# Optimization experiments

Hardware: AMD Instinct MI355X
Metric: run time of the kernel (lower is better)

## Reference

```python
import jax, jax.numpy as jnp
import numpy as np

NUM_HEADS = 16

def rotate_half(x):
    x1, x2 = jnp.split(x, 2, axis=-1)
    return jnp.concatenate((-x2, x1), axis=-1)

def setup_inputs() -> dict:
    key = jax.random.key(0)
    ks = jax.random.split(key, 5)
    b, n, dim, hd = 2, 2048, 1024, 64
    return {
        "x": jax.random.normal(ks[0], (b, n, dim), dtype=jnp.float32),
        "Wqkv": jax.random.normal(ks[1], (3 * dim, dim), dtype=jnp.float32) * (dim ** -0.5),
        "Wproj": jax.random.normal(ks[2], (dim, dim), dtype=jnp.float32) * (dim ** -0.5),
        "bproj": jnp.zeros((dim,), dtype=jnp.float32),
        "sin": jax.random.normal(ks[3], (n, hd), dtype=jnp.float32),
        "cos": jax.random.normal(ks[4], (n, hd), dtype=jnp.float32),
    }

def reference(x, Wqkv, Wproj, bproj, sin, cos):
    b, n, dim = x.shape
    h = NUM_HEADS
    d = dim // h
    qkv = x @ Wqkv.T
    qkv = qkv.reshape(b, n, 3, h, d).transpose(2, 0, 3, 1, 4)
    q, k, v = qkv[0], qkv[1], qkv[2]
    # RoPE: sin/cos [n, d] broadcast over [b, h, n, d]
    q = q * cos + rotate_half(q) * sin
    k = k * cos + rotate_half(k) * sin
    # SDPA (non-causal, no dropout at eval)
    scale = d ** -0.5
    scores = jnp.einsum("bhnd,bhmd->bhnm", q, k) * scale
    attn = jax.nn.softmax(scores, axis=-1)
    out = jnp.einsum("bhnm,bhmd->bhnd", attn, v)
    # merge heads: [b, h, n, d] -> [b, n, h*d]
    out = out.transpose(0, 2, 1, 3).reshape(b, n, dim)
    return out @ Wproj.T + bproj
```

## Files before the change

### kernel.cpp

```cpp
#include <hip/hip_runtime.h>
#include <hip/hip_fp16.h>

typedef _Float16 f16;
typedef _Float16 half8 __attribute__((ext_vector_type(8)));
typedef _Float16 half4v __attribute__((ext_vector_type(4)));
typedef __fp16 fp16x2 __attribute__((ext_vector_type(2)));
typedef float f32x4 __attribute__((ext_vector_type(4)));

#define QSCALE 0.18033688011112042f
#define SHIFT2 17.312340490667560f

__device__ __forceinline__ void gload_lds16(const void* g, void* lds) {
  __builtin_amdgcn_global_load_lds(
      (__attribute__((address_space(1))) void*)g,
      (__attribute__((address_space(3))) void*)lds, 16, 0, 0);
}

__global__ __launch_bounds__(256) void cvt_all_kernel(
    const float* __restrict__ x, const float* __restrict__ wqkv,
    const float* __restrict__ wproj, f16* __restrict__ xh,
    f16* __restrict__ wqkvh, f16* __restrict__ wprojh) {
  int i = blockIdx.x * 256 + threadIdx.x;
  const float* src; f16* dst; int off;
  if (i < 1048576)      { src = x;     dst = xh;     off = i; }
  else if (i < 1835008) { src = wqkv;  dst = wqkvh;  off = i - 1048576; }
  else                  { src = wproj; dst = wprojh; off = i - 1835008; }
  float4 v = ((const float4*)src)[off];
  half4v o;
  o.x = (f16)v.x; o.y = (f16)v.y; o.z = (f16)v.z; o.w = (f16)v.w;
  ((half4v*)dst)[off] = o;
}

template<int EPI, int VAR>
__global__ __launch_bounds__(256) void hgemm_kernel(
    const f16* __restrict__ A16, const f16* __restrict__ B, int K, int yoff,
    const float* __restrict__ cosT, const float* __restrict__ sinT,
    f16* __restrict__ Qout, f16* __restrict__ Kout, f16* __restrict__ Vtout,
    const float* __restrict__ bias, float* __restrict__ Cout) {
  constexpr int BN = (EPI == 0) ? 128 : 64;
  constexpr int NJ = (EPI == 0) ? 4 : 2;
  constexpr int NBUF = (VAR == 0) ? 2 : 3;
  __shared__ f16 As[NBUF][128 * 32];
  __shared__ f16 Bs[NBUF][BN * 32];
  const int tid = threadIdx.x;
  const int lane = tid & 63, w = tid >> 6;
  const int fr = lane & 15, fkg = lane >> 4;
  const int wm = (w >> 1) * 64;
  const int wn = (EPI == 0) ? (w & 1) * 64 : (w & 1) * 16;
  const long long rowBase = (long long)blockIdx.x * 128;
  const long long colBase = (long long)(blockIdx.y + yoff) * BN;

  f32x4 acc[4][NJ] = {};
  const f16* Ab = A16 + rowBase * K;
  const f16* Bb = B + colBase * K;

  const int srow = lane >> 2;
  const int kcol = ((lane & 3) ^ ((lane >> 3) & 3)) * 8;
  const int sw = (fkg ^ ((fr >> 1) & 3)) * 8;

  auto stage = [&](int buf, int k0) {
#pragma unroll
    for (int r = 0; r < 2; ++r) {
      int c = r * 4 + w;
      gload_lds16(Ab + (long long)(c * 16 + srow) * K + k0 + kcol, &As[buf][c * 512]);
    }
    if (EPI == 0) {
#pragma unroll
      for (int r = 0; r < 2; ++r) {
        int c = r * 4 + w;
        gload_lds16(Bb + (long long)(c * 16 + srow) * K + k0 + kcol, &Bs[buf][c * 512]);
      }
    } else {
      int c = w;
      gload_lds16(Bb + (long long)(c * 16 + srow) * K + k0 + kcol, &Bs[buf][c * 512]);
    }
  };

  const int NT = K >> 5;
  stage(0, 0);
  stage(1, 32);
  if (VAR == 0) {
    for (int t = 0; t < NT; ++t) {
      const int buf = t & 1;
      const int k0 = t << 5;
      if (t + 1 < NT) {
        if constexpr (EPI == 0) asm volatile("s_waitcnt vmcnt(4)" ::: "memory");
        else                    asm volatile("s_waitcnt vmcnt(3)" ::: "memory");
      } else {
        asm volatile("s_waitcnt vmcnt(0)" ::: "memory");
      }
      __builtin_amdgcn_s_barrier();
      __builtin_amdgcn_sched_barrier(0);
      half8 a[4], b[NJ];
#pragma unroll
      for (int i = 0; i < 4; ++i)
        a[i] = *(const half8*)(&As[buf][((wm >> 4) + i) * 512 + fr * 32 + sw]);
#pragma unroll
      for (int j = 0; j < NJ; ++j) {
        int chunk = (EPI == 0) ? ((wn >> 4) + j) : ((wn >> 4) + j * 2);
        b[j] = *(const half8*)(&Bs[buf][chunk * 512 + fr * 32 + sw]);
      }
      asm volatile("s_waitcnt lgkmcnt(0)" ::: "memory");
      __builtin_amdgcn_sched_barrier(0);
      __builtin_amdgcn_s_barrier();
      if (t + 2 < NT) stage(buf, k0 + 64);
#pragma unroll
      for (int i = 0; i < 4; ++i)
#pragma unroll
        for (int j = 0; j < NJ; ++j)
          acc[i][j] = __builtin_amdgcn_mfma_f32_16x16x32_f16(a[i], b[j], acc[i][j], 0, 0, 0);
    }
  } else {
    int bcur = 0, bst = 2;
    for (int t = 0; t < NT; ++t) {
      if (t + 1 < NT) {
        if constexpr (EPI == 0) asm volatile("s_waitcnt vmcnt(4)" ::: "memory");
        else                    asm volatile("s_waitcnt vmcnt(3)" ::: "memory");
      } else {
        asm volatile("s_waitcnt vmcnt(0)" ::: "memory");
      }
      __builtin_amdgcn_s_barrier();
      __builtin_amdgcn_sched_barrier(0);
      if (t + 2 < NT) stage(bst, (t + 2) << 5);
      half8 a[4], b[NJ];
#pragma unroll
      for (int i = 0; i < 4; ++i)
        a[i] = *(const half8*)(&As[bcur][((wm >> 4) + i) * 512 + fr * 32 + sw]);
#pragma unroll
      for (int j = 0; j < NJ; ++j) {
        int chunk = (EPI == 0) ? ((wn >> 4) + j) : ((wn >> 4) + j * 2);
        b[j] = *(const half8*)(&Bs[bcur][chunk * 512 + fr * 32 + sw]);
      }
#pragma unroll
      for (int i = 0; i < 4; ++i)
#pragma unroll
        for (int j = 0; j < NJ; ++j)
          acc[i][j] = __builtin_amdgcn_mfma_f32_16x16x32_f16(a[i], b[j], acc[i][j], 0, 0, 0);
      bcur = (bcur == 2) ? 0 : bcur + 1;
      bst  = (bst == 2) ? 0 : bst + 1;
    }
  }

  if (EPI == 0) {
#pragma unroll
    for (int i = 0; i < 4; ++i) {
#pragma unroll
      for (int r = 0; r < 4; ++r) {
        int rg = (int)rowBase + wm + i * 16 + fkg * 4 + r;
        int bidx = rg >> 11, nn = rg & 2047;
#pragma unroll
        for (int j = 0; j < 4; ++j) {
          int cg = (int)colBase + wn + j * 16 + fr;
          int t = cg >> 10, cc = cg & 1023;
          int head = cc >> 6, d = cc & 63;
          int bh = bidx * 16 + head;
          float v = acc[i][j][r];
          if (t == 2) {
            Vtout[((long long)bh * 64 + d) * 2048 + nn] = (f16)v;
          } else {
            float pal = acc[i][j ^ 2][r];
            float cs = cosT[nn * 64 + d];
            float sn = sinT[nn * 64 + d];
            v = v * cs + (d < 32 ? -pal : pal) * sn;
            if (t == 0) v *= QSCALE;
            f16 hv = (f16)v;
            if (t == 0) Qout[((long long)bh * 2048 + nn) * 64 + d] = hv;
            else        Kout[((long long)bh * 2048 + nn) * 64 + d] = hv;
          }
        }
      }
    }
  } else {
#pragma unroll
    for (int i = 0; i < 4; ++i)
#pragma unroll
      for (int r = 0; r < 4; ++r) {
        long long rg = rowBase + wm + i * 16 + fkg * 4 + r;
#pragma unroll
        for (int j = 0; j < NJ; ++j) {
          int cg = (int)colBase + wn + j * 32 + fr;
          Cout[rg * 1024 + cg] = acc[i][j][r] + bias[cg];
        }
      }
  }
}

__global__ __launch_bounds__(256) void attn_kernel(
    const f16* __restrict__ Q, const f16* __restrict__ Kb,
    const f16* __restrict__ Vt, f16* __restrict__ Om) {
  __shared__ f16 Ks[2][64 * 64];
  __shared__ f16 Vs[2][64 * 64];
  const int tid = threadIdx.x;
  const int lane = tid & 63, w = tid >> 6;
  const int fr = lane & 15, fkg = lane >> 4, fk = fkg * 8;

  const int lin = blockIdx.x;
  const int slot = lin >> 3;
  const int bh = (lin & 7) * 4 + (slot >> 4);
  const int q0 = (slot & 15) * 128 + w * 32;

  const f16* Kbh = Kb + (long long)bh * 2048 * 64;
  const f16* Vbh = Vt + (long long)bh * 64 * 2048;

  half8 aq[2][2];
#pragma unroll
  for (int m = 0; m < 2; ++m)
#pragma unroll
    for (int ks = 0; ks < 2; ++ks)
      aq[m][ks] = *(const half8*)(Q + ((long long)bh * 2048 + q0 + m * 16 + fr) * 64 +
                                  ks * 32 + fk);

  half8 ones_frag;
#pragma unroll
  for (int j = 0; j < 8; ++j) ones_frag[j] = (fr == 0) ? (f16)1.0f : (f16)0.0f;

  f32x4 acc[2][4] = {};
  f32x4 accL[2] = {};

  const int srow = lane >> 3;
  const int ssub = ((lane & 7) ^ srow) * 8;
  long long koff[2], voff[2];
  int ldst[2];
#pragma unroll
  for (int c = 0; c < 2; ++c) {
    int R = w * 16 + c * 8 + srow;
    int pr = (R & 0x23) | ((R & 0x0C) << 1) | ((R & 0x10) >> 2);
    koff[c] = (long long)pr * 64 + ssub;
    voff[c] = (long long)R * 2048 + ssub;
    ldst[c] = (w * 16 + c * 8) * 64;
  }
  const f16* kpt = Kbh;
  const f16* vpt = Vbh;

  auto stage = [&](int buf) {
#pragma unroll
    for (int c = 0; c < 2; ++c) {
      gload_lds16(kpt + koff[c], &Ks[buf][ldst[c]]);
      gload_lds16(vpt + voff[c], &Vs[buf][ldst[c]]);
    }
    kpt += 4096;
    vpt += 64;
  };

  stage(0);
  stage(1);

  const float negshift = -SHIFT2;
  auto body = [&](int t, int buf) {
    if (t < 31) asm volatile("s_waitcnt vmcnt(4)" ::: "memory");
    else        asm volatile("s_waitcnt vmcnt(0)" ::: "memory");
    __builtin_amdgcn_s_barrier();
    __builtin_amdgcn_sched_barrier(0);

    f32x4 z[2][4];
#pragma unroll
    for (int n = 0; n < 4; ++n) {
      half8 bk0 = *(const half8*)(&Ks[buf][(n * 16 + fr) * 64 + ((fkg ^ (fr & 7)) * 8)]);
      half8 bk1 = *(const half8*)(&Ks[buf][(n * 16 + fr) * 64 + (((4 | fkg) ^ (fr & 7)) * 8)]);
#pragma unroll
      for (int m = 0; m < 2; ++m) {
        f32x4 tz = {negshift, negshift, negshift, negshift};
        tz = __builtin_amdgcn_mfma_f32_16x16x32_f16(bk0, aq[m][0], tz, 0, 0, 0);
        tz = __builtin_amdgcn_mfma_f32_16x16x32_f16(bk1, aq[m][1], tz, 0, 0, 0);
        z[m][n] = tz;
      }
    }

    half8 av[2][4];
#pragma unroll
    for (int ks = 0; ks < 2; ++ks)
#pragma unroll
      for (int dd = 0; dd < 4; ++dd)
        av[ks][dd] = *(const half8*)(&Vs[buf][(dd * 16 + fr) * 64 +
                                              ((((ks << 2) | fkg) ^ (fr & 7)) * 8)]);

    half8 ap[2][2];
#pragma unroll
    for (int m = 0; m < 2; ++m)
#pragma unroll
      for (int ks = 0; ks < 2; ++ks) {
        union { half8 v; fp16x2 p[4]; } u;
        u.p[0] = __builtin_amdgcn_cvt_pkrtz(
            __builtin_amdgcn_exp2f(z[m][2 * ks][0]),
            __builtin_amdgcn_exp2f(z[m][2 * ks][1]));
        u.p[1] = __builtin_amdgcn_cvt_pkrtz(
            __builtin_amdgcn_exp2f(z[m][2 * ks][2]),
            __builtin_amdgcn_exp2f(z[m][2 * ks][3]));
        u.p[2] = __builtin_amdgcn_cvt_pkrtz(
            __builtin_amdgcn_exp2f(z[m][2 * ks + 1][0]),
            __builtin_amdgcn_exp2f(z[m][2 * ks + 1][1]));
        u.p[3] = __builtin_amdgcn_cvt_pkrtz(
            __builtin_amdgcn_exp2f(z[m][2 * ks + 1][2]),
            __builtin_amdgcn_exp2f(z[m][2 * ks + 1][3]));
        ap[m][ks] = u.v;
      }

#pragma unroll
    for (int ks = 0; ks < 2; ++ks) {
#pragma unroll
      for (int m = 0; m < 2; ++m)
        accL[m] = __builtin_amdgcn_mfma_f32_16x16x32_f16(ones_frag, ap[m][ks], accL[m], 0, 0, 0);
#pragma unroll
      for (int dd = 0; dd < 4; ++dd)
#pragma unroll
        for (int m = 0; m < 2; ++m)
          acc[m][dd] = __builtin_amdgcn_mfma_f32_16x16x32_f16(av[ks][dd], ap[m][ks], acc[m][dd], 0, 0, 0);
    }

    asm volatile("s_waitcnt lgkmcnt(0)" ::: "memory");
    __builtin_amdgcn_sched_barrier(0);
    __builtin_amdgcn_s_barrier();
    if (t < 30) stage(buf);
  };

  for (int t = 0; t < 32; t += 2) {
    body(t, 0);
    body(t + 1, 1);
  }

  const int b = bh >> 4, h = bh & 15;
#pragma unroll
  for (int m = 0; m < 2; ++m) {
    float l = __shfl(accL[m][0], fr);
    float inv = 1.f / l;
#pragma unroll
    for (int dd = 0; dd < 4; ++dd) {
      half4v o;
#pragma unroll
      for (int r = 0; r < 4; ++r) o[r] = (f16)(acc[m][dd][r] * inv);
      *(half4v*)(&Om[((long long)b * 2048 + q0 + m * 16 + fr) * 1024 +
                     h * 64 + dd * 16 + fkg * 4]) = o;
    }
  }
}

extern "C" void kernel_launch(void* const* d_in, const int* in_sizes, int n_in,
                              void* d_out, int out_size, void* d_ws, size_t ws_size,
                              hipStream_t stream) {
  (void)in_sizes; (void)n_in; (void)out_size; (void)ws_size;
  const float* x     = (const float*)d_in[0];
  const float* Wqkv  = (const float*)d_in[1];
  const float* Wproj = (const float*)d_in[2];
  const float* bproj = (const float*)d_in[3];
  const float* sinT  = (const float*)d_in[4];
  const float* cosT  = (const float*)d_in[5];
  float* out = (float*)d_out;

  f16* ws     = (f16*)d_ws;
  f16* xh     = ws;
  f16* Om     = ws;
  f16* Wqkvh  = ws + 4194304;
  f16* Wprojh = ws + 7340032;
  f16* Qb     = ws + 8388608;
  f16* Kb     = ws + 12582912;
  f16* Vtb    = ws + 16777216;

  cvt_all_kernel<<<8192, 256, 0, stream>>>(x, Wqkv, Wproj, xh, Wqkvh, Wprojh);

  hgemm_kernel<0, 1><<<dim3(32, 24), 256, 0, stream>>>(
      xh, Wqkvh, 1024, 0, cosT, sinT, Qb, Kb, Vtb, nullptr, nullptr);

  attn_kernel<<<512, 256, 0, stream>>>(Qb, Kb, Vtb, Om);

  hgemm_kernel<1, 0><<<dim3(32, 16), 256, 0, stream>>>(
      Om, Wprojh, 1024, 0, nullptr, nullptr, nullptr, nullptr, nullptr, bproj, out);
}
```

Measured before the change: 121.2 us.

## Replace QKV GEMM with 256x256-tile, 8-wave kernel and XCD-aware block mapping

```diff
diff --git a/kernel.cpp b/kernel.cpp
--- a/kernel.cpp
+++ b/kernel.cpp
@@ -31,26 +31,174 @@
   ((half4v*)dst)[off] = o;
 }
 
-template<int EPI, int VAR>
-__global__ __launch_bounds__(256) void hgemm_kernel(
-    const f16* __restrict__ A16, const f16* __restrict__ B, int K, int yoff,
+__global__ __launch_bounds__(512, 1) void hgemm8p_kernel(
+    const f16* __restrict__ A16, const f16* __restrict__ B,
     const float* __restrict__ cosT, const float* __restrict__ sinT,
-    f16* __restrict__ Qout, f16* __restrict__ Kout, f16* __restrict__ Vtout,
+    f16* __restrict__ Qout, f16* __restrict__ Kout, f16* __restrict__ Vtout) {
+  constexpr int K = 1024;
+  __shared__ f16 As[2][256 * 64];
+  __shared__ f16 Bs[2][256 * 64];
+  const int tid = threadIdx.x;
+  const int lane = tid & 63, w = tid >> 6;
+  const int fr = lane & 15, fkg = lane >> 4;
+  const int wr = w >> 2, wc = w & 3;
+
+  const int lin = blockIdx.x;
+  const int wgid = (lin & 7) * 24 + (lin >> 3);
+  const int bm = wgid / 12, bn = wgid % 12;
+  const long long rowBase = (long long)bm * 256;
+  const long long colBase = (long long)bn * 256;
+
+  f32x4 acc[8][4] = {};
+  const f16* Ab = A16 + rowBase * K;
+  const f16* Bb = B + colBase * K;
+
+  int srow[2], scol[2], sdst[2];
+#pragma unroll
+  for (int p = 0; p < 2; ++p) {
+    int slot = p * 512 + tid;
+    int row = slot >> 3, sd = slot & 7;
+    srow[p] = row;
+    scol[p] = (sd ^ (row & 7)) * 8;
+    sdst[p] = row * 64 + sd * 8;
+  }
+
+  auto stageTile = [&](int buf, int k0) {
+#pragma unroll
+    for (int p = 0; p < 2; ++p) {
+      gload_lds16(Ab + (long long)srow[p] * K + k0 + scol[p], &As[buf][sdst[p]]);
+      gload_lds16(Ab + (long long)(128 + srow[p]) * K + k0 + scol[p],
+                  &As[buf][128 * 64 + sdst[p]]);
+      gload_lds16(Bb + (long long)srow[p] * K + k0 + scol[p], &Bs[buf][sdst[p]]);
+      gload_lds16(Bb + (long long)(128 + srow[p]) * K + k0 + scol[p],
+                  &Bs[buf][128 * 64 + sdst[p]]);
+    }
+  };
+
+  const int arow = wr * 128 + fr;
+  const int brow = wc * 64 + fr;
+  const int sub0 = ((0 + fkg) ^ (fr & 7)) * 8;
+  const int sub1 = ((4 + fkg) ^ (fr & 7)) * 8;
+
+  stageTile(0, 0);
+  for (int t = 0; t < 16; ++t) {
+    const int buf = t & 1;
+    asm volatile("s_waitcnt vmcnt(0)" ::: "memory");
+    __builtin_amdgcn_s_barrier();
+    __builtin_amdgcn_sched_barrier(0);
+    if (t + 1 < 16) stageTile(buf ^ 1, (t + 1) << 6);
+
+    half8 a[4][2], b0[2][2], b1[2][2];
+#pragma unroll
+    for (int i = 0; i < 4; ++i) {
+      a[i][0] = *(const half8*)(&As[buf][(arow + i * 16) * 64 + sub0]);
+      a[i][1] = *(const half8*)(&As[buf][(arow + i * 16) * 64 + sub1]);
+    }
+#pragma unroll
+    for (int j = 0; j < 2; ++j) {
+      b0[j][0] = *(const half8*)(&Bs[buf][(brow + j * 16) * 64 + sub0]);
+      b0[j][1] = *(const half8*)(&Bs[buf][(brow + j * 16) * 64 + sub1]);
+    }
+    __builtin_amdgcn_s_setprio(1);
+#pragma unroll
+    for (int i = 0; i < 4; ++i)
+#pragma unroll
+      for (int j = 0; j < 2; ++j)
+#pragma unroll
+        for (int kk = 0; kk < 2; ++kk)
+          acc[i][j] = __builtin_amdgcn_mfma_f32_16x16x32_f16(a[i][kk], b0[j][kk], acc[i][j], 0, 0, 0);
+    __builtin_amdgcn_s_setprio(0);
+    __builtin_amdgcn_s_barrier();
+#pragma unroll
+    for (int j = 0; j < 2; ++j) {
+      b1[j][0] = *(const half8*)(&Bs[buf][(brow + (j + 2) * 16) * 64 + sub0]);
+      b1[j][1] = *(const half8*)(&Bs[buf][(brow + (j + 2) * 16) * 64 + sub1]);
+    }
+    __builtin_amdgcn_s_setprio(1);
+#pragma unroll
+    for (int i = 0; i < 4; ++i)
+#pragma unroll
+      for (int j = 0; j < 2; ++j)
+#pragma unroll
+        for (int kk = 0; kk < 2; ++kk)
+          acc[i][j + 2] = __builtin_amdgcn_mfma_f32_16x16x32_f16(a[i][kk], b1[j][kk], acc[i][j + 2], 0, 0, 0);
+    __builtin_amdgcn_s_setprio(0);
+    __builtin_amdgcn_s_barrier();
+#pragma unroll
+    for (int i = 0; i < 4; ++i) {
+      a[i][0] = *(const half8*)(&As[buf][(arow + (i + 4) * 16) * 64 + sub0]);
+      a[i][1] = *(const half8*)(&As[buf][(arow + (i + 4) * 16) * 64 + sub1]);
+    }
+    __builtin_amdgcn_s_setprio(1);
+#pragma unroll
+    for (int i = 0; i < 4; ++i)
+#pragma unroll
+      for (int j = 0; j < 2; ++j)
+#pragma unroll
+        for (int kk = 0; kk < 2; ++kk)
+          acc[i + 4][j] = __builtin_amdgcn_mfma_f32_16x16x32_f16(a[i][kk], b0[j][kk], acc[i + 4][j], 0, 0, 0);
+    __builtin_amdgcn_s_setprio(0);
+    __builtin_amdgcn_s_barrier();
+    __builtin_amdgcn_s_setprio(1);
+#pragma unroll
+    for (int i = 0; i < 4; ++i)
+#pragma unroll
+      for (int j = 0; j < 2; ++j)
+#pragma unroll
+        for (int kk = 0; kk < 2; ++kk)
+          acc[i + 4][j + 2] = __builtin_amdgcn_mfma_f32_16x16x32_f16(a[i][kk], b1[j][kk], acc[i + 4][j + 2], 0, 0, 0);
+    __builtin_amdgcn_s_setprio(0);
+  }
+
+  const int cb0 = (int)colBase + wc * 64;
+  const int tcol = cb0 >> 10;
+  const int head = (cb0 & 1023) >> 6;
+#pragma unroll
+  for (int i = 0; i < 8; ++i) {
+#pragma unroll
+    for (int r = 0; r < 4; ++r) {
+      int rg = (int)rowBase + wr * 128 + i * 16 + fkg * 4 + r;
+      int bidx = rg >> 11, nn = rg & 2047;
+      int bh = bidx * 16 + head;
+      if (tcol == 2) {
+#pragma unroll
+        for (int j = 0; j < 4; ++j) {
+          int d = j * 16 + fr;
+          Vtout[((long long)bh * 64 + d) * 2048 + nn] = (f16)acc[i][j][r];
+        }
+      } else {
+#pragma unroll
+        for (int j = 0; j < 4; ++j) {
+          int d = j * 16 + fr;
+          float v = acc[i][j][r];
+          float pal = acc[i][j ^ 2][r];
+          float cs = cosT[nn * 64 + d];
+          float sn = sinT[nn * 64 + d];
+          v = v * cs + (d < 32 ? -pal : pal) * sn;
+          if (tcol == 0) v *= QSCALE;
+          f16 hv = (f16)v;
+          if (tcol == 0) Qout[((long long)bh * 2048 + nn) * 64 + d] = hv;
+          else           Kout[((long long)bh * 2048 + nn) * 64 + d] = hv;
+        }
+      }
+    }
+  }
+}
+
+__global__ __launch_bounds__(256) void hgemm_out_kernel(
+    const f16* __restrict__ A16, const f16* __restrict__ B, int K,
     const float* __restrict__ bias, float* __restrict__ Cout) {
-  constexpr int BN = (EPI == 0) ? 128 : 64;
-  constexpr int NJ = (EPI == 0) ? 4 : 2;
-  constexpr int NBUF = (VAR == 0) ? 2 : 3;
-  __shared__ f16 As[NBUF][128 * 32];
-  __shared__ f16 Bs[NBUF][BN * 32];
+  __shared__ f16 As[2][128 * 32];
+  __shared__ f16 Bs[2][64 * 32];
   const int tid = threadIdx.x;
   const int lane = tid & 63, w = tid >> 6;
   const int fr = lane & 15, fkg = lane >> 4;
   const int wm = (w >> 1) * 64;
-  const int wn = (EPI == 0) ? (w & 1) * 64 : (w & 1) * 16;
+  const int wn = (w & 1) * 16;
   const long long rowBase = (long long)blockIdx.x * 128;
-  const long long colBase = (long long)(blockIdx.y + yoff) * BN;
-
-  f32x4 acc[4][NJ] = {};
+  const long long colBase = (long long)blockIdx.y * 64;
+
+  f32x4 acc[4][2] = {};
   const f16* Ab = A16 + rowBase * K;
   const f16* Bb = B + colBase * K;
 
@@ -64,125 +212,49 @@
       int c = r * 4 + w;
       gload_lds16(Ab + (long long)(c * 16 + srow) * K + k0 + kcol, &As[buf][c * 512]);
     }
-    if (EPI == 0) {
-#pragma unroll
-      for (int r = 0; r < 2; ++r) {
-        int c = r * 4 + w;
-        gload_lds16(Bb + (long long)(c * 16 + srow) * K + k0 + kcol, &Bs[buf][c * 512]);
-      }
-    } else {
-      int c = w;
-      gload_lds16(Bb + (long long)(c * 16 + srow) * K + k0 + kcol, &Bs[buf][c * 512]);
-    }
+    int c = w;
+    gload_lds16(Bb + (long long)(c * 16 + srow) * K + k0 + kcol, &Bs[buf][c * 512]);
   };
 
   const int NT = K >> 5;
   stage(0, 0);
   stage(1, 32);
-  if (VAR == 0) {
-    for (int t = 0; t < NT; ++t) {
-      const int buf = t & 1;
-      const int k0 = t << 5;
-      if (t + 1 < NT) {
-        if constexpr (EPI == 0) asm volatile("s_waitcnt vmcnt(4)" ::: "memory");
-        else                    asm volatile("s_waitcnt vmcnt(3)" ::: "memory");
-      } else {
-        asm volatile("s_waitcnt vmcnt(0)" ::: "memory");
+  for (int t = 0; t < NT; ++t) {
+    const int buf = t & 1;
+    const int k0 = t << 5;
+    if (t + 1 < NT) asm volatile("s_waitcnt vmcnt(3)" ::: "memory");
+    else            asm volatile("s_waitcnt vmcnt(0)" ::: "memory");
+    __builtin_amdgcn_s_barrier();
+    __builtin_amdgcn_sched_barrier(0);
+    half8 a[4], b[2];
+#pragma unroll
+    for (int i = 0; i < 4; ++i)
+      a[i] = *(const half8*)(&As[buf][((wm >> 4) + i) * 512 + fr * 32 + sw]);
+#pragma unroll
+    for (int j = 0; j < 2; ++j)
+      b[j] = *(const half8*)(&Bs[buf][((wn >> 4) + j * 2) * 512 + fr * 32 + sw]);
+    asm volatile("s_waitcnt lgkmcnt(0)" ::: "memory");
+    __builtin_amdgcn_sched_barrier(0);
+    __builtin_amdgcn_s_barrier();
+    if (t + 2 < NT) stage(buf, k0 + 64);
+#pragma unroll
+    for (int i = 0; i < 4; ++i)
+#pragma unroll
+      for (int j = 0; j < 2; ++j)
+        acc[i][j] = __builtin_amdgcn_mfma_f32_16x16x32_f16(a[i], b[j], acc[i][j], 0, 0, 0);
+  }
+
+#pragma unroll
+  for (int i = 0; i < 4; ++i)
+#pragma unroll
+    for (int r = 0; r < 4; ++r) {
+      long long rg = rowBase + wm + i * 16 + fkg * 4 + r;
+#pragma unroll
+      for (int j = 0; j < 2; ++j) {
+        int cg = (int)colBase + wn + j * 32 + fr;
+        Cout[rg * 1024 + cg] = acc[i][j][r] + bias[cg];
       }
-      __builtin_amdgcn_s_barrier();
-      __builtin_amdgcn_sched_barrier(0);
-      half8 a[4], b[NJ];
-#pragma unroll
-      for (int i = 0; i < 4; ++i)
-        a[i] = *(const half8*)(&As[buf][((wm >> 4) + i) * 512 + fr * 32 + sw]);
-#pragma unroll
-      for (int j = 0; j < NJ; ++j) {
-        int chunk = (EPI == 0) ? ((wn >> 4) + j) : ((wn >> 4) + j * 2);
-        b[j] = *(const half8*)(&Bs[buf][chunk * 512 + fr * 32 + sw]);
-      }
-      asm volatile("s_waitcnt lgkmcnt(0)" ::: "memory");
-      __builtin_amdgcn_sched_barrier(0);
-      __builtin_amdgcn_s_barrier();
-      if (t + 2 < NT) stage(buf, k0 + 64);
-#pragma unroll
-      for (int i = 0; i < 4; ++i)
-#pragma unroll
-        for (int j = 0; j < NJ; ++j)
-          acc[i][j] = __builtin_amdgcn_mfma_f32_16x16x32_f16(a[i], b[j], acc[i][j], 0, 0, 0);
-    }
-  } else {
-    int bcur = 0, bst = 2;
-    for (int t = 0; t < NT; ++t) {
-      if (t + 1 < NT) {
-        if constexpr (EPI == 0) asm volatile("s_waitcnt vmcnt(4)" ::: "memory");
-        else                    asm volatile("s_waitcnt vmcnt(3)" ::: "memory");
-      } else {
-        asm volatile("s_waitcnt vmcnt(0)" ::: "memory");
-      }
-      __builtin_amdgcn_s_barrier();
-      __builtin_amdgcn_sched_barrier(0);
-      if (t + 2 < NT) stage(bst, (t + 2) << 5);
-      half8 a[4], b[NJ];
-#pragma unroll
-      for (int i = 0; i < 4; ++i)
-        a[i] = *(const half8*)(&As[bcur][((wm >> 4) + i) * 512 + fr * 32 + sw]);
-#pragma unroll
-      for (int j = 0; j < NJ; ++j) {
-        int chunk = (EPI == 0) ? ((wn >> 4) + j) : ((wn >> 4) + j * 2);
-        b[j] = *(const half8*)(&Bs[bcur][chunk * 512 + fr * 32 + sw]);
-      }
-#pragma unroll
-      for (int i = 0; i < 4; ++i)
-#pragma unroll
-        for (int j = 0; j < NJ; ++j)
-          acc[i][j] = __builtin_amdgcn_mfma_f32_16x16x32_f16(a[i], b[j], acc[i][j], 0, 0, 0);
-      bcur = (bcur == 2) ? 0 : bcur + 1;
-      bst  = (bst == 2) ? 0 : bst + 1;
-    }
-  }
-
-  if (EPI == 0) {
-#pragma unroll
-    for (int i = 0; i < 4; ++i) {
-#pragma unroll
-      for (int r = 0; r < 4; ++r) {
-        int rg = (int)rowBase + wm + i * 16 + fkg * 4 + r;
-        int bidx = rg >> 11, nn = rg & 2047;
-#pragma unroll
-        for (int j = 0; j < 4; ++j) {
-          int cg = (int)colBase + wn + j * 16 + fr;
-          int t = cg >> 10, cc = cg & 1023;
-          int head = cc >> 6, d = cc & 63;
-          int bh = bidx * 16 + head;
-          float v = acc[i][j][r];
-          if (t == 2) {
-            Vtout[((long long)bh * 64 + d) * 2048 + nn] = (f16)v;
-          } else {
-            float pal = acc[i][j ^ 2][r];
-            float cs = cosT[nn * 64 + d];
-            float sn = sinT[nn * 64 + d];
-            v = v * cs + (d < 32 ? -pal : pal) * sn;
-            if (t == 0) v *= QSCALE;
-            f16 hv = (f16)v;
-            if (t == 0) Qout[((long long)bh * 2048 + nn) * 64 + d] = hv;
-            else        Kout[((long long)bh * 2048 + nn) * 64 + d] = hv;
-          }
-        }
-      }
-    }
-  } else {
-#pragma unroll
-    for (int i = 0; i < 4; ++i)
-#pragma unroll
-      for (int r = 0; r < 4; ++r) {
-        long long rg = rowBase + wm + i * 16 + fkg * 4 + r;
-#pragma unroll
-        for (int j = 0; j < NJ; ++j) {
-          int cg = (int)colBase + wn + j * 32 + fr;
-          Cout[rg * 1024 + cg] = acc[i][j][r] + bias[cg];
-        }
-      }
-  }
+    }
 }
 
 __global__ __launch_bounds__(256) void attn_kernel(
@@ -357,11 +429,11 @@
 
   cvt_all_kernel<<<8192, 256, 0, stream>>>(x, Wqkv, Wproj, xh, Wqkvh, Wprojh);
 
-  hgemm_kernel<0, 1><<<dim3(32, 24), 256, 0, stream>>>(
-      xh, Wqkvh, 1024, 0, cosT, sinT, Qb, Kb, Vtb, nullptr, nullptr);
+  hgemm8p_kernel<<<192, 512, 0, stream>>>(
+      xh, Wqkvh, cosT, sinT, Qb, Kb, Vtb);
 
   attn_kernel<<<512, 256, 0, stream>>>(Qb, Kb, Vtb, Om);
 
-  hgemm_kernel<1, 0><<<dim3(32, 16), 256, 0, stream>>>(
-      Om, Wprojh, 1024, 0, nullptr, nullptr, nullptr, nullptr, nullptr, bproj, out);
-}
+  hgemm_out_kernel<<<dim3(32, 16), 256, 0, stream>>>(
+      Om, Wprojh, 1024, bproj, out);
+}
```

Measured after the change: 133.9 us. 10.5% more time.
